# Kernel tuning notes

Measured on AMD Instinct MI355X. Metric: run time of the kernel, lower is better.

The kernel has to match this reference:

```python
import jax, jax.numpy as jnp
import numpy as np

M = 8192      # nodes
D = 128       # feature dim
DEG = 32      # neighbors per node


def setup_inputs() -> dict:
    key = jax.random.key(0)
    ks = jax.random.split(key, 6)
    z = jax.random.normal(ks[0], (M, D), dtype=jnp.float32)
    # deterministic, duplicate-free edge list: node i -> (i+1..i+DEG) mod M
    src = jnp.repeat(jnp.arange(M, dtype=jnp.int64), DEG)
    dst = (src + jnp.tile(jnp.arange(1, DEG + 1, dtype=jnp.int64), M)) % M
    edge_index = jnp.stack([src, dst], axis=0)  # [2, M*DEG]
    s = 1.0 / np.sqrt(D)
    Wg = jax.random.normal(ks[1], (D, D), dtype=jnp.float32) * s
    Wc = jax.random.normal(ks[2], (D, D), dtype=jnp.float32) * s
    Wq = jax.random.normal(ks[3], (D, D), dtype=jnp.float32) * s
    Wk = jax.random.normal(ks[4], (D, D), dtype=jnp.float32) * s
    a = jax.random.normal(ks[5], (2 * D,), dtype=jnp.float32)
    return {"z": z, "edge_index": edge_index, "Wg": Wg, "Wc": Wc,
            "Wq": Wq, "Wk": Wk, "a": a}


def reference(z, edge_index, Wg, Wc, Wq, Wk, a):
    m, d = z.shape
    wg = z @ Wg.T                              # [m, d]
    src, dst = edge_index[0], edge_index[1]
    a_src, a_dst = a[:d], a[d:]
    # per-edge score: leaky_relu(a . [wg[i], wg[j]]) = leaky_relu(a1.wg[i] + a2.wg[j])
    scores = jax.nn.leaky_relu((wg @ a_src)[src] + (wg @ a_dst)[dst])  # [E]
    # softmax over each source node's neighbors (segment softmax)
    smax = jax.ops.segment_max(scores, src, num_segments=m)
    ex = jnp.exp(scores - smax[src])
    denom = jax.ops.segment_sum(ex, src, num_segments=m)
    alpha = ex / denom[src]                    # [E]
    # scatter-aggregate: local[i] = sum_j alpha_ij * wg[j]
    local = jax.ops.segment_sum(alpha[:, None] * wg[dst], src, num_segments=m)
    # dense global attention branch
    q = z @ Wq.T
    k = z @ Wk.T
    beta = jax.nn.softmax(q @ k.T / jnp.sqrt(jnp.float32(d)), axis=-1)  # [m, m]
    global_msg = beta @ (z @ Wc.T)
    return jax.nn.leaky_relu(local + global_msg + z)
```

## Files before the change

kernel.cpp:

```cpp
#include <hip/hip_runtime.h>

#define MM 8192
#define DD 128
#define DEG 32
#define KSPLIT 8
#define BK 64
#define NTILE 16
#define NB 16
#define RSTAGE 48

typedef __attribute__((ext_vector_type(8))) _Float16 h8;
typedef __attribute__((ext_vector_type(4))) float f4;
typedef __attribute__((ext_vector_type(4))) unsigned int u4;

__device__ __forceinline__ unsigned short f2h(float f) {
  _Float16 h = (_Float16)f;
  return __builtin_bit_cast(unsigned short, h);
}

__device__ __forceinline__ unsigned int pkrtz(float a, float b) {
  return __builtin_bit_cast(unsigned int, __builtin_amdgcn_cvt_pkrtz(a, b));
}

__device__ __forceinline__ void lds_dma16(const unsigned short* gptr, unsigned short* lptr) {
  __builtin_amdgcn_global_load_lds(
      (const __attribute__((address_space(1))) unsigned int*)gptr,
      (__attribute__((address_space(3))) unsigned int*)lptr, 16, 0, 0);
}

__global__ __launch_bounds__(256) void proj_kernel(
    const float* __restrict__ z, const float* __restrict__ Wg,
    const float* __restrict__ Wc, const float* __restrict__ Wq,
    const float* __restrict__ Wk, const float* __restrict__ a,
    float* __restrict__ wg, unsigned short* __restrict__ qb,
    unsigned short* __restrict__ kb, unsigned short* __restrict__ ct,
    float* __restrict__ sg, float* __restrict__ sd)
{
  __shared__ unsigned short zt[64 * 136];
  __shared__ unsigned short wt[128 * 136];
  const int mode = blockIdx.y;
  const float* __restrict__ W = (mode == 0) ? Wg : (mode == 1) ? Wq : (mode == 2) ? Wk : Wc;
  const int r0 = blockIdx.x * 64;
  const int tid = threadIdx.x;

  #pragma unroll
  for (int it = 0; it < 8; ++it) {
    int id = tid + it * 256, row = id >> 5, c4 = (id & 31) * 4;
    f4 v = *(const f4*)(z + (r0 + row) * DD + c4);
    uint2 pk; pk.x = pkrtz(v.x, v.y); pk.y = pkrtz(v.z, v.w);
    *(uint2*)&zt[row * 136 + c4] = pk;
  }
  #pragma unroll
  for (int it = 0; it < 16; ++it) {
    int id = tid + it * 256, row = id >> 5, c4 = (id & 31) * 4;
    f4 v = *(const f4*)(W + row * DD + c4);
    uint2 pk; pk.x = pkrtz(v.x, v.y); pk.y = pkrtz(v.z, v.w);
    *(uint2*)&wt[row * 136 + c4] = pk;
  }
  __syncthreads();

  const int lane = tid & 63, w = tid >> 6, n = lane & 15, quad = lane >> 4;
  h8 afr[4];
  #pragma unroll
  for (int kt = 0; kt < 4; ++kt)
    afr[kt] = *(const h8*)&zt[(16 * w + n) * 136 + kt * 32 + quad * 8];

  f4 acc[8];
  const f4 fzero = {0.f, 0.f, 0.f, 0.f};
  #pragma unroll
  for (int nt = 0; nt < 8; ++nt) {
    f4 c = fzero;
    #pragma unroll
    for (int kt = 0; kt < 4; ++kt) {
      h8 b = *(const h8*)&wt[(16 * nt + n) * 136 + kt * 32 + quad * 8];
      c = __builtin_amdgcn_mfma_f32_16x16x32_f16(afr[kt], b, c, 0, 0, 0);
    }
    acc[nt] = c;
  }

  if (mode == 0) {
    #pragma unroll
    for (int nt = 0; nt < 8; ++nt)
      #pragma unroll
      for (int r = 0; r < 4; ++r)
        wg[(r0 + 16 * w + quad * 4 + r) * DD + 16 * nt + n] = acc[nt][r];
    float av[8], bv[8];
    #pragma unroll
    for (int nt = 0; nt < 8; ++nt) { av[nt] = a[16 * nt + n]; bv[nt] = a[DD + 16 * nt + n]; }
    #pragma unroll
    for (int r = 0; r < 4; ++r) {
      float s1 = 0.f, s2 = 0.f;
      #pragma unroll
      for (int nt = 0; nt < 8; ++nt) { s1 += acc[nt][r] * av[nt]; s2 += acc[nt][r] * bv[nt]; }
      s1 += __shfl_xor(s1, 1); s1 += __shfl_xor(s1, 2); s1 += __shfl_xor(s1, 4); s1 += __shfl_xor(s1, 8);
      s2 += __shfl_xor(s2, 1); s2 += __shfl_xor(s2, 2); s2 += __shfl_xor(s2, 4); s2 += __shfl_xor(s2, 8);
      if (n == 0) {
        int g = r0 + 16 * w + quad * 4 + r;
        sg[g] = s1; sd[g] = s2;
      }
    }
  } else if (mode == 1) {
    const float qscale = 0.08838834764831845f;
    #pragma unroll
    for (int nt = 0; nt < 8; ++nt)
      #pragma unroll
      for (int r = 0; r < 4; ++r)
        qb[(r0 + 16 * w + quad * 4 + r) * DD + 16 * nt + n] = f2h(acc[nt][r] * qscale);
  } else if (mode == 2) {
    #pragma unroll
    for (int nt = 0; nt < 8; ++nt)
      #pragma unroll
      for (int r = 0; r < 4; ++r)
        kb[(r0 + 16 * w + quad * 4 + r) * DD + 16 * nt + n] = f2h(acc[nt][r]);
  } else {
    __syncthreads();
    #pragma unroll
    for (int nt = 0; nt < 8; ++nt)
      #pragma unroll
      for (int r = 0; r < 4; ++r)
        wt[(16 * nt + n) * 80 + 16 * w + quad * 4 + r] = f2h(acc[nt][r]);
    __syncthreads();
    #pragma unroll
    for (int it = 0; it < 4; ++it) {
      int idx = tid + it * 256, d = idx >> 3, c8 = (idx & 7) * 8;
      u4 v = *(const u4*)&wt[d * 80 + c8];
      *(u4*)(ct + (size_t)d * MM + r0 + c8) = v;
    }
  }
}

__global__ __launch_bounds__(512, 2) void flash_kernel(
    const unsigned short* __restrict__ qb, const unsigned short* __restrict__ kb,
    const unsigned short* __restrict__ ct, unsigned short* __restrict__ Opart,
    float* __restrict__ Lpart)
{
  __shared__ unsigned short sh[41984];
  const int bx = blockIdx.x, ck = blockIdx.y;
  const int tid = threadIdx.x, lane = tid & 63, w = tid >> 6;
  const int n = lane & 15, quad = lane >> 4;
  const int ln = n, lq = quad;
  const int qr0 = bx * 256;

  #pragma unroll
  for (int it = 0; it < 8; ++it)
    lds_dma16(qb + (qr0 + (it * 2 + (w >> 2)) * 16 + ln) * DD + (w & 3) * 32 + lq * 8,
              &sh[(it * 512 + tid) * 8]);
  __syncthreads();
  h8 aq[2][4];
  #pragma unroll
  for (int mt = 0; mt < 2; ++mt)
    #pragma unroll
    for (int kt = 0; kt < 4; ++kt)
      aq[mt][kt] = *(const h8*)&sh[((w * 2 + mt) * 4 + kt) * 512 + lane * 8];
  __syncthreads();

  const unsigned short* kp = kb + (size_t)(ck * 1024 + 4 * ln + (w >> 2)) * DD + (w & 3) * 32 + lq * 8;
  const unsigned short* vp = ct + (size_t)(16 * (w >> 1) + ln) * MM + ck * 1024 + (w & 1) * 32 + lq * 8;

  #pragma unroll
  for (int j = 0; j < 2; ++j)
    lds_dma16(kp + j * 2 * DD, &sh[(j * 512 + tid) * 8]);
  #pragma unroll
  for (int j = 0; j < 2; ++j)
    lds_dma16(vp + (size_t)j * 64 * MM, &sh[8192 + (j * 512 + tid) * 8]);

  f4 acc_o[2][8];
  const f4 fzero = {0.f, 0.f, 0.f, 0.f};
  #pragma unroll
  for (int mt = 0; mt < 2; ++mt)
    #pragma unroll
    for (int dt = 0; dt < 8; ++dt) acc_o[mt][dt] = fzero;
  float l_r[2][4] = {{0.f, 0.f, 0.f, 0.f}, {0.f, 0.f, 0.f, 0.f}};
  const int pbase = 32768 + w * 1152;

  for (int t = 0; t < NTILE; ++t) {
    __syncthreads();
    const int cur = (t & 1) * 16384;

    if (t < NTILE - 1) {
      const int nb = ((t + 1) & 1) * 16384;
      const unsigned short* kpn = kp + (size_t)(t + 1) * BK * DD;
      const unsigned short* vpn = vp + (t + 1) * BK;
      #pragma unroll
      for (int j = 0; j < 2; ++j)
        lds_dma16(kpn + j * 2 * DD, &sh[nb + (j * 512 + tid) * 8]);
      #pragma unroll
      for (int j = 0; j < 2; ++j)
        lds_dma16(vpn + (size_t)j * 64 * MM, &sh[nb + 8192 + (j * 512 + tid) * 8]);
    }

    f4 accs[2][4];
    #pragma unroll
    for (int mt = 0; mt < 2; ++mt)
      #pragma unroll
      for (int nt = 0; nt < 4; ++nt) accs[mt][nt] = fzero;
    #pragma unroll
    for (int nt = 0; nt < 4; ++nt) {
      #pragma unroll
      for (int kt = 0; kt < 4; ++kt) {
        h8 bk = *(const h8*)&sh[cur + nt * 2048 + kt * 512 + lane * 8];
        accs[0][nt] = __builtin_amdgcn_mfma_f32_16x16x32_f16(aq[0][kt], bk, accs[0][nt], 0, 0, 0);
        accs[1][nt] = __builtin_amdgcn_mfma_f32_16x16x32_f16(aq[1][kt], bk, accs[1][nt], 0, 0, 0);
      }
    }

    h8 ap[2][2];
    #pragma unroll
    for (int mt = 0; mt < 2; ++mt) {
      #pragma unroll
      for (int r = 0; r < 4; ++r) {
        float p0 = __expf(fminf(accs[mt][0][r], 10.f));
        float p1 = __expf(fminf(accs[mt][1][r], 10.f));
        float p2 = __expf(fminf(accs[mt][2][r], 10.f));
        float p3 = __expf(fminf(accs[mt][3][r], 10.f));
        l_r[mt][r] += (p0 + p1) + (p2 + p3);
        uint2 pv; pv.x = pkrtz(p0, p1); pv.y = pkrtz(p2, p3);
        *(uint2*)&sh[pbase + (quad * 4 + r) * 72 + n * 4] = pv;
      }
      ap[mt][0] = *(const h8*)&sh[pbase + n * 72 + quad * 8];
      ap[mt][1] = *(const h8*)&sh[pbase + n * 72 + 32 + quad * 8];
    }

    #pragma unroll
    for (int dt = 0; dt < 8; ++dt) {
      #pragma unroll
      for (int k2 = 0; k2 < 2; ++k2) {
        h8 bv = *(const h8*)&sh[cur + 8192 + dt * 1024 + k2 * 512 + lane * 8];
        acc_o[0][dt] = __builtin_amdgcn_mfma_f32_16x16x32_f16(ap[0][k2], bv, acc_o[0][dt], 0, 0, 0);
        acc_o[1][dt] = __builtin_amdgcn_mfma_f32_16x16x32_f16(ap[1][k2], bv, acc_o[1][dt], 0, 0, 0);
      }
    }
  }

  #pragma unroll
  for (int mt = 0; mt < 2; ++mt)
    #pragma unroll
    for (int r = 0; r < 4; ++r) {
      float lv = l_r[mt][r];
      lv += __shfl_xor(lv, 1); lv += __shfl_xor(lv, 2);
      lv += __shfl_xor(lv, 4); lv += __shfl_xor(lv, 8);
      int g = qr0 + w * 32 + mt * 16 + quad * 4 + r;
      if (n == 0) Lpart[ck * MM + g] = lv;
      #pragma unroll
      for (int dt = 0; dt < 8; ++dt)
        Opart[((size_t)ck * MM + g) * DD + 16 * dt + n] = f2h(acc_o[mt][dt][r]);
    }
}

__global__ __launch_bounds__(256) void merge_kernel(
    const int* __restrict__ ei, const float* __restrict__ wg,
    const float* __restrict__ sg, const float* __restrict__ sd,
    const unsigned short* __restrict__ Opart, const float* __restrict__ Lpart,
    const float* __restrict__ z, float* __restrict__ out)
{
  __shared__ float rows_s[RSTAGE * 132];
  __shared__ float sc_s[NB][DEG];
  __shared__ float alpha_s[NB][DEG];
  __shared__ int idx_s[NB][DEG];
  const int tid = threadIdx.x;
  const int i0 = blockIdx.x * NB;

  #pragma unroll
  for (int it = 0; it < 6; ++it) {
    int idx = tid + it * 256;
    int r = idx >> 5, c4 = (idx & 31) * 4;
    int grow = (i0 + 1 + r) & (MM - 1);
    *(f4*)&rows_s[r * 132 + c4] = *(const f4*)(wg + (size_t)grow * DD + c4);
  }
  #pragma unroll
  for (int it = 0; it < 2; ++it) {
    int e = tid + it * 256;
    int nj = e >> 5, j = e & 31;
    int i = i0 + nj;
    int dstj = ei[MM * DEG + i * DEG + j];
    float s = sg[i] + sd[dstj];
    sc_s[nj][j] = s > 0.f ? s : 0.01f * s;
    idx_s[nj][j] = (dstj - (i0 + 1)) & (MM - 1);
  }
  __syncthreads();

  const int ni = tid >> 4, l16 = tid & 15;
  {
    float s0 = sc_s[ni][l16], s1 = sc_s[ni][l16 + 16];
    float mx = fmaxf(s0, s1);
    mx = fmaxf(mx, __shfl_xor(mx, 1)); mx = fmaxf(mx, __shfl_xor(mx, 2));
    mx = fmaxf(mx, __shfl_xor(mx, 4)); mx = fmaxf(mx, __shfl_xor(mx, 8));
    float p0 = __expf(s0 - mx), p1 = __expf(s1 - mx);
    float sum = p0 + p1;
    sum += __shfl_xor(sum, 1); sum += __shfl_xor(sum, 2);
    sum += __shfl_xor(sum, 4); sum += __shfl_xor(sum, 8);
    float inv = 1.f / sum;
    alpha_s[ni][l16] = p0 * inv;
    alpha_s[ni][l16 + 16] = p1 * inv;
  }

  const int d0 = l16 * 8;
  const int i = i0 + ni;
  f4 a0 = {0.f, 0.f, 0.f, 0.f}, a1 = {0.f, 0.f, 0.f, 0.f};
  #pragma unroll 4
  for (int j = 0; j < DEG; ++j) {
    float al = alpha_s[ni][j];
    int r = idx_s[ni][j];
    const f4* src = (r < RSTAGE)
        ? (const f4*)&rows_s[r * 132 + d0]
        : (const f4*)(wg + (size_t)((i0 + 1 + r) & (MM - 1)) * DD + d0);
    f4 v0 = src[0], v1 = src[1];
    a0 += v0 * al;
    a1 += v1 * al;
  }

  float l = 0.f;
  float o[8] = {0.f, 0.f, 0.f, 0.f, 0.f, 0.f, 0.f, 0.f};
  #pragma unroll
  for (int ck = 0; ck < KSPLIT; ++ck) {
    l += Lpart[ck * MM + i];
    h8 v = *(const h8*)(Opart + ((size_t)ck * MM + i) * DD + d0);
    #pragma unroll
    for (int q = 0; q < 8; ++q) o[q] += (float)v[q];
  }
  float inv = 1.0f / l;
  const float* zp = z + (size_t)i * DD + d0;
  float* op = out + (size_t)i * DD + d0;
  #pragma unroll
  for (int q = 0; q < 8; ++q) {
    float ac = (q < 4) ? a0[q] : a1[q - 4];
    float r = o[q] * inv + ac + zp[q];
    op[q] = r > 0.f ? r : 0.01f * r;
  }
}

extern "C" void kernel_launch(void* const* d_in, const int* in_sizes, int n_in,
                              void* d_out, int out_size, void* d_ws, size_t ws_size,
                              hipStream_t stream) {
  const float* z  = (const float*)d_in[0];
  const int*   ei = (const int*)d_in[1];
  const float* Wg = (const float*)d_in[2];
  const float* Wc = (const float*)d_in[3];
  const float* Wq = (const float*)d_in[4];
  const float* Wk = (const float*)d_in[5];
  const float* a  = (const float*)d_in[6];
  float* out = (float*)d_out;
  char* ws = (char*)d_ws;

  float*          wg    = (float*)(ws + 0);
  unsigned short* qb    = (unsigned short*)(ws + (4 << 20));
  unsigned short* kb    = (unsigned short*)(ws + (6 << 20));
  unsigned short* ct    = (unsigned short*)(ws + (8 << 20));
  float*          sg    = (float*)(ws + (10 << 20));
  float*          sd    = (float*)(ws + (10 << 20) + (64 << 10));
  unsigned short* Opart = (unsigned short*)(ws + (11 << 20));
  float*          Lpart = (float*)(ws + (27 << 20));

  proj_kernel<<<dim3(128, 4), 256, 0, stream>>>(z, Wg, Wc, Wq, Wk, a, wg, qb, kb, ct, sg, sd);
  flash_kernel<<<dim3(32, KSPLIT), 512, 0, stream>>>(qb, kb, ct, Opart, Lpart);
  merge_kernel<<<512, 256, 0, stream>>>(ei, wg, sg, sd, Opart, Lpart, z, out);
}
```

Baseline: 119.9 us.

## Software-pipeline attention loop so PV of previous tile overlaps QK of current

Restructures the flash-attention style inner loop into a skewed pipeline. Each iteration now issues the QK MFMAs for tile t and the PV MFMAs for tile t-1 back to back, and the K and V tile loads are staggered so V for tile t arrives one step later. The goal is to hide the softmax exp and LDS round-trip latency behind independent matrix work. In exchange it needs a prologue and epilogue and holds the accs and ap registers live across iterations, which raises register pressure.

```diff
diff --git a/kernel.cpp b/kernel.cpp
--- a/kernel.cpp
+++ b/kernel.cpp
@@ -160,11 +160,10 @@
   #pragma unroll
   for (int j = 0; j < 2; ++j)
     lds_dma16(kp + j * 2 * DD, &sh[(j * 512 + tid) * 8]);
-  #pragma unroll
-  for (int j = 0; j < 2; ++j)
-    lds_dma16(vp + (size_t)j * 64 * MM, &sh[8192 + (j * 512 + tid) * 8]);
 
   f4 acc_o[2][8];
+  f4 accs[2][4];
+  h8 ap[2][2];
   const f4 fzero = {0.f, 0.f, 0.f, 0.f};
   #pragma unroll
   for (int mt = 0; mt < 2; ++mt)
@@ -173,64 +172,82 @@
   float l_r[2][4] = {{0.f, 0.f, 0.f, 0.f}, {0.f, 0.f, 0.f, 0.f}};
   const int pbase = 32768 + w * 1152;
 
-  for (int t = 0; t < NTILE; ++t) {
+#define QK_TILE(CUR)                                                          \
+  { accs[0][0] = fzero; accs[0][1] = fzero; accs[0][2] = fzero; accs[0][3] = fzero; \
+    accs[1][0] = fzero; accs[1][1] = fzero; accs[1][2] = fzero; accs[1][3] = fzero; \
+    _Pragma("unroll")                                                         \
+    for (int nt = 0; nt < 4; ++nt) {                                          \
+      _Pragma("unroll")                                                       \
+      for (int kt = 0; kt < 4; ++kt) {                                        \
+        h8 bk = *(const h8*)&sh[(CUR) + nt * 2048 + kt * 512 + lane * 8];     \
+        accs[0][nt] = __builtin_amdgcn_mfma_f32_16x16x32_f16(aq[0][kt], bk, accs[0][nt], 0, 0, 0); \
+        accs[1][nt] = __builtin_amdgcn_mfma_f32_16x16x32_f16(aq[1][kt], bk, accs[1][nt], 0, 0, 0); \
+      }                                                                       \
+    } }
+
+#define PV_TILE(PRV)                                                          \
+  { _Pragma("unroll")                                                         \
+    for (int dt = 0; dt < 8; ++dt) {                                          \
+      _Pragma("unroll")                                                       \
+      for (int k2 = 0; k2 < 2; ++k2) {                                        \
+        h8 bv = *(const h8*)&sh[(PRV) + 8192 + dt * 1024 + k2 * 512 + lane * 8]; \
+        acc_o[0][dt] = __builtin_amdgcn_mfma_f32_16x16x32_f16(ap[0][k2], bv, acc_o[0][dt], 0, 0, 0); \
+        acc_o[1][dt] = __builtin_amdgcn_mfma_f32_16x16x32_f16(ap[1][k2], bv, acc_o[1][dt], 0, 0, 0); \
+      }                                                                       \
+    } }
+
+#define SOFTMAX_TILE                                                          \
+  { _Pragma("unroll")                                                         \
+    for (int mt = 0; mt < 2; ++mt) {                                          \
+      _Pragma("unroll")                                                       \
+      for (int r = 0; r < 4; ++r) {                                           \
+        float p0 = __expf(fminf(accs[mt][0][r], 10.f));                       \
+        float p1 = __expf(fminf(accs[mt][1][r], 10.f));                       \
+        float p2 = __expf(fminf(accs[mt][2][r], 10.f));                       \
+        float p3 = __expf(fminf(accs[mt][3][r], 10.f));                       \
+        l_r[mt][r] += (p0 + p1) + (p2 + p3);                                  \
+        uint2 pv; pv.x = pkrtz(p0, p1); pv.y = pkrtz(p2, p3);                 \
+        *(uint2*)&sh[pbase + (quad * 4 + r) * 72 + n * 4] = pv;               \
+      }                                                                       \
+      ap[mt][0] = *(const h8*)&sh[pbase + n * 72 + quad * 8];                 \
+      ap[mt][1] = *(const h8*)&sh[pbase + n * 72 + 32 + quad * 8];            \
+    } }
+
+  __syncthreads();
+  #pragma unroll
+  for (int j = 0; j < 2; ++j)
+    lds_dma16(kp + (size_t)BK * DD + j * 2 * DD, &sh[16384 + (j * 512 + tid) * 8]);
+  #pragma unroll
+  for (int j = 0; j < 2; ++j)
+    lds_dma16(vp + (size_t)j * 64 * MM, &sh[8192 + (j * 512 + tid) * 8]);
+  QK_TILE(0)
+  SOFTMAX_TILE
+
+  for (int t = 1; t < NTILE; ++t) {
     __syncthreads();
     const int cur = (t & 1) * 16384;
+    const int prv = cur ^ 16384;
 
     if (t < NTILE - 1) {
-      const int nb = ((t + 1) & 1) * 16384;
       const unsigned short* kpn = kp + (size_t)(t + 1) * BK * DD;
-      const unsigned short* vpn = vp + (t + 1) * BK;
       #pragma unroll
       for (int j = 0; j < 2; ++j)
-        lds_dma16(kpn + j * 2 * DD, &sh[nb + (j * 512 + tid) * 8]);
+        lds_dma16(kpn + j * 2 * DD, &sh[prv + (j * 512 + tid) * 8]);
+    }
+    {
+      const unsigned short* vpn = vp + t * BK;
       #pragma unroll
       for (int j = 0; j < 2; ++j)
-        lds_dma16(vpn + (size_t)j * 64 * MM, &sh[nb + 8192 + (j * 512 + tid) * 8]);
-    }
-
-    f4 accs[2][4];
-    #pragma unroll
-    for (int mt = 0; mt < 2; ++mt)
-      #pragma unroll
-      for (int nt = 0; nt < 4; ++nt) accs[mt][nt] = fzero;
-    #pragma unroll
-    for (int nt = 0; nt < 4; ++nt) {
-      #pragma unroll
-      for (int kt = 0; kt < 4; ++kt) {
-        h8 bk = *(const h8*)&sh[cur + nt * 2048 + kt * 512 + lane * 8];
-        accs[0][nt] = __builtin_amdgcn_mfma_f32_16x16x32_f16(aq[0][kt], bk, accs[0][nt], 0, 0, 0);
-        accs[1][nt] = __builtin_amdgcn_mfma_f32_16x16x32_f16(aq[1][kt], bk, accs[1][nt], 0, 0, 0);
-      }
-    }
-
-    h8 ap[2][2];
-    #pragma unroll
-    for (int mt = 0; mt < 2; ++mt) {
-      #pragma unroll
-      for (int r = 0; r < 4; ++r) {
-        float p0 = __expf(fminf(accs[mt][0][r], 10.f));
-        float p1 = __expf(fminf(accs[mt][1][r], 10.f));
-        float p2 = __expf(fminf(accs[mt][2][r], 10.f));
-        float p3 = __expf(fminf(accs[mt][3][r], 10.f));
-        l_r[mt][r] += (p0 + p1) + (p2 + p3);
-        uint2 pv; pv.x = pkrtz(p0, p1); pv.y = pkrtz(p2, p3);
-        *(uint2*)&sh[pbase + (quad * 4 + r) * 72 + n * 4] = pv;
-      }
-      ap[mt][0] = *(const h8*)&sh[pbase + n * 72 + quad * 8];
-      ap[mt][1] = *(const h8*)&sh[pbase + n * 72 + 32 + quad * 8];
-    }
-
-    #pragma unroll
-    for (int dt = 0; dt < 8; ++dt) {
-      #pragma unroll
-      for (int k2 = 0; k2 < 2; ++k2) {
-        h8 bv = *(const h8*)&sh[cur + 8192 + dt * 1024 + k2 * 512 + lane * 8];
-        acc_o[0][dt] = __builtin_amdgcn_mfma_f32_16x16x32_f16(ap[0][k2], bv, acc_o[0][dt], 0, 0, 0);
-        acc_o[1][dt] = __builtin_amdgcn_mfma_f32_16x16x32_f16(ap[1][k2], bv, acc_o[1][dt], 0, 0, 0);
-      }
-    }
-  }
+        lds_dma16(vpn + (size_t)j * 64 * MM, &sh[cur + 8192 + (j * 512 + tid) * 8]);
+    }
+
+    QK_TILE(cur)
+    PV_TILE(prv)
+    SOFTMAX_TILE
+  }
+
+  __syncthreads();
+  PV_TILE(16384)
 
   #pragma unroll
   for (int mt = 0; mt < 2; ++mt)
@@ -245,6 +262,9 @@
       for (int dt = 0; dt < 8; ++dt)
         Opart[((size_t)ck * MM + g) * DD + 16 * dt + n] = f2h(acc_o[mt][dt][r]);
     }
+#undef QK_TILE
+#undef PV_TILE
+#undef SOFTMAX_TILE
 }
 
 __global__ __launch_bounds__(256) void merge_kernel(
```

Measured after the change: 123.0 us. 1.03x slower.
